# Kernel optimization log

Hardware: AMD Instinct MI355X
Metric: run time of the kernel (lower is better)

Reference implementation:

```python
import jax, jax.numpy as jnp
import numpy as np

D_MODEL = 1024
N_HEADS = 16


def setup_inputs() -> dict:
    key = jax.random.key(0)
    ks = jax.random.split(key, 5)
    B, L, D = 2, 2048, D_MODEL
    x = jax.random.normal(ks[0], (B, L, D), dtype=jnp.float32)
    # Linear params (torch nn.Linear: y = x @ W.T + b); store as (in, out) for einsum.
    s_attn = 1.0 / np.sqrt(D)
    W_attn = jax.random.uniform(ks[1], (D, 3 * D), jnp.float32, -s_attn, s_attn)
    b_attn = jax.random.uniform(ks[2], (3 * D,), jnp.float32, -s_attn, s_attn)
    W_proj = jax.random.uniform(ks[3], (D, D), jnp.float32, -s_attn, s_attn)
    b_proj = jax.random.uniform(ks[4], (D,), jnp.float32, -s_attn, s_attn)
    return {"x": x, "W_attn": W_attn, "b_attn": b_attn, "W_proj": W_proj, "b_proj": b_proj}


def reference(x, W_attn, b_attn, W_proj, b_proj):
    B, L, D = x.shape
    H = N_HEADS
    hd = D // H
    qkv = jnp.einsum('bld,de->ble', x, W_attn) + b_attn  # [B,L,3D]
    # Faithful to source bug: q and v are both taken from the k projection.
    k_lin = qkv[:, :, D:2 * D]
    k = k_lin.reshape(B, L, H, hd).transpose(0, 2, 1, 3)  # [B,H,L,hd]
    q = k
    v = k
    att = jnp.einsum('bhqd,bhkd->bhqk', q, k) / jnp.sqrt(jnp.float32(hd))
    att = jax.nn.softmax(att, axis=3)
    out = jnp.einsum('bhqk,bhkd->bhqd', att, v)  # [B,H,L,hd]
    out = out.transpose(0, 2, 1, 3).reshape(B, L, D)
    return jnp.einsum('bld,de->ble', out, W_proj) + b_proj
```

## Files before the change

### kernel.cpp

```cpp
#include <hip/hip_runtime.h>
#include <hip/hip_bf16.h>

typedef __attribute__((ext_vector_type(8))) short short8;
typedef __attribute__((ext_vector_type(4))) float f32x4;
typedef __attribute__((ext_vector_type(16))) float f32x16;
typedef unsigned short u16;
typedef unsigned int u32;

static __device__ __forceinline__ u16 f2b(float f) {
  __hip_bfloat16 h = __float2bfloat16(f);
  return __builtin_bit_cast(u16, h);
}
static __device__ __forceinline__ float b2f(u16 v) {
  return __builtin_bit_cast(float, ((u32)v) << 16);
}
static __device__ __forceinline__ u32 pk2(float lo, float hi) {
  return (u32)f2b(lo) | ((u32)f2b(hi) << 16);
}
static __device__ __forceinline__ u32 cvtpk(float lo, float hi) {
  u32 r;
  asm("v_cvt_pk_bf16_f32 %0, %1, %2" : "=v"(r) : "v"(lo), "v"(hi));
  return r;
}

static __device__ __forceinline__ void gload16(const void* g, void* l) {
  __builtin_amdgcn_global_load_lds((const __attribute__((address_space(1))) void*)g,
                                   (__attribute__((address_space(3))) void*)l, 16, 0, 0);
}

static __device__ __forceinline__ void barrier_fenced() {
  __builtin_amdgcn_sched_barrier(0);
  asm volatile("" ::: "memory");
  __builtin_amdgcn_s_barrier();
  __builtin_amdgcn_sched_barrier(0);
  asm volatile("" ::: "memory");
}

__global__ __launch_bounds__(256) void prep(const float4* __restrict__ x4,
                                            uint2* __restrict__ xb,
                                            const float* __restrict__ W_attn,
                                            u16* __restrict__ Wkt,
                                            const float* __restrict__ W_proj,
                                            u16* __restrict__ Wpt) {
  __shared__ u16 tile[32][33];
  int bid = blockIdx.x, t = threadIdx.x;
  if (bid < 4096) {
    int i = bid * 256 + t;
    float4 v = x4[i];
    uint2 o;
    o.x = pk2(v.x, v.y);
    o.y = pk2(v.z, v.w);
    xb[i] = o;
    return;
  }
  const float* in;
  u16* out;
  int in_rs, col_off, blk;
  if (bid < 5120) {
    in = W_attn; out = Wkt; in_rs = 3072; col_off = 1024; blk = bid - 4096;
  } else {
    in = W_proj; out = Wpt; in_rs = 1024; col_off = 0; blk = bid - 5120;
  }
  int tx = t & 31, ty = t >> 5;
  int r0 = (blk >> 5) * 32, c0 = (blk & 31) * 32;
#pragma unroll
  for (int i = 0; i < 4; ++i) {
    int r = r0 + ty + i * 8;
    tile[ty + i * 8][tx] = f2b(in[(size_t)r * in_rs + col_off + c0 + tx]);
  }
  __syncthreads();
#pragma unroll
  for (int i = 0; i < 4; ++i) {
    int c = c0 + ty + i * 8;
    out[(size_t)c * 1024 + r0 + tx] = tile[tx][ty + i * 8];
  }
}

__global__ __launch_bounds__(256) void transpose_heads(const u16* __restrict__ in,
                                                       u16* __restrict__ out) {
  __shared__ u16 tile[32][33];
  int t = threadIdx.x, tx = t & 31, ty = t >> 5;
  int r0 = (blockIdx.x >> 5) * 32;
  int c0 = (blockIdx.x & 31) * 32;
#pragma unroll
  for (int i = 0; i < 4; ++i)
    tile[ty + i * 8][tx] = in[(size_t)(r0 + ty + i * 8) * 1024 + c0 + tx];
  __syncthreads();
  int r = r0 + tx;
  int b = r >> 11;
#pragma unroll
  for (int i = 0; i < 4; ++i) {
    int c = c0 + ty + i * 8;
    out[((size_t)(b * 1024 + c) << 11) + (r & 2047)] = tile[tx][ty + i * 8];
  }
}

template <bool OUT_F32>
__global__ __launch_bounds__(256) void gemm_bias(const u16* __restrict__ A,
                                                 const u16* __restrict__ Bt,
                                                 const float* __restrict__ bias,
                                                 void* __restrict__ Cp, int M, int N, int K) {
  __shared__ char lds[3][24576];
  int tid = threadIdx.x, lane = tid & 63, wid = tid >> 6;
  int lr = lane & 15, lh = lane >> 4;
  int p = blockIdx.x;
  int m0 = (p >> 3) << 6, n0 = (p & 7) << 7;
  int wm = wid >> 1, wn = wid & 1;
  f32x4 acc[2][4] = {};
  int srow = lane >> 3;
  int scol = ((lane & 7) << 4) ^ (srow << 4);
  const char* Ab = (const char*)A;
  const char* Bb = (const char*)Bt;
  int r0 = wid * 8;
  const int NT = K >> 6;

  auto stage = [&](char* buf, int k0) {
    char* lA = buf;
    char* lB = buf + 8192;
    gload16(Ab + ((size_t)(m0 + r0 + srow) * K + k0) * 2 + scol, lA + r0 * 128);
    gload16(Ab + ((size_t)(m0 + 32 + r0 + srow) * K + k0) * 2 + scol, lA + (32 + r0) * 128);
#pragma unroll
    for (int i = 0; i < 4; ++i)
      gload16(Bb + ((size_t)(n0 + i * 32 + r0 + srow) * K + k0) * 2 + scol,
              lB + (i * 32 + r0) * 128);
  };

  stage(lds[0], 0);
  stage(lds[1], 64);
  for (int t = 0; t < NT; ++t) {
    if (t + 1 < NT)
      asm volatile("s_waitcnt vmcnt(6) lgkmcnt(0)" ::: "memory");
    else
      asm volatile("s_waitcnt vmcnt(0) lgkmcnt(0)" ::: "memory");
    barrier_fenced();
    char* lA = lds[t % 3];
    char* lB = lA + 8192;
    short8 af[2][2], bfr[4][2];
#pragma unroll
    for (int mi = 0; mi < 2; ++mi)
#pragma unroll
      for (int ks = 0; ks < 2; ++ks) {
        int row = wm * 32 + mi * 16 + lr;
        af[mi][ks] = *(const short8*)(lA + row * 128 + ((ks * 64 + lh * 16) ^ ((row & 7) << 4)));
      }
#pragma unroll
    for (int ni = 0; ni < 4; ++ni)
#pragma unroll
      for (int ks = 0; ks < 2; ++ks) {
        int row = wn * 64 + ni * 16 + lr;
        bfr[ni][ks] = *(const short8*)(lB + row * 128 + ((ks * 64 + lh * 16) ^ ((row & 7) << 4)));
      }
    __builtin_amdgcn_s_setprio(1);
#pragma unroll
    for (int ks = 0; ks < 2; ++ks)
#pragma unroll
      for (int mi = 0; mi < 2; ++mi)
#pragma unroll
        for (int ni = 0; ni < 4; ++ni)
          acc[mi][ni] = __builtin_amdgcn_mfma_f32_16x16x32_bf16(af[mi][ks], bfr[ni][ks],
                                                                acc[mi][ni], 0, 0, 0);
    __builtin_amdgcn_s_setprio(0);
    if (t + 2 < NT) stage(lds[(t + 2) % 3], (t + 2) << 6);
  }
#pragma unroll
  for (int mi = 0; mi < 2; ++mi)
#pragma unroll
    for (int ni = 0; ni < 4; ++ni) {
      int col = n0 + wn * 64 + ni * 16 + lr;
      float bz = bias[col];
#pragma unroll
      for (int r = 0; r < 4; ++r) {
        int row = m0 + wm * 32 + mi * 16 + lh * 4 + r;
        float v = acc[mi][ni][r] + bz;
        if (OUT_F32)
          ((float*)Cp)[(size_t)row * N + col] = v;
        else
          ((u16*)Cp)[(size_t)row * N + col] = f2b(v);
      }
    }
}

__global__ __launch_bounds__(256) void flash_attn(const u16* __restrict__ Kb,
                                                  const u16* __restrict__ Kt,
                                                  u16* __restrict__ AO) {
  __shared__ char kv[3][16384];
  const float S2 = 0.125f * 1.44269504088896340736f;
  int tid = threadIdx.x, lane = tid & 63, wid = tid >> 6;
  int ql = lane & 31, half = lane >> 5;
  int rb = blockIdx.x;
  int bid = (rb & 7) * 64 + (rb >> 3);
  int qb = bid & 15, h = (bid >> 4) & 15, b = bid >> 8;
  int qbase = b * 2048 + qb * 128 + wid * 32;
  int hc = h * 64;
  short8 qfr[4];
#pragma unroll
  for (int ds = 0; ds < 4; ++ds) {
    short8 raw = *(const short8*)(Kb + (size_t)(qbase + ql) * 1024 + hc + ds * 16 + half * 8);
    short8 q;
#pragma unroll
    for (int j = 0; j < 8; ++j) q[j] = (short)f2b(b2f((u16)raw[j]) * S2);
    qfr[ds] = q;
  }
  const short8 ones = {0x3F80, 0x3F80, 0x3F80, 0x3F80, 0x3F80, 0x3F80, 0x3F80, 0x3F80};
  f32x16 acc0 = {}, acc1 = {}, accs = {};
  int srow = lane >> 3;
  int scol = ((lane & 7) << 4) ^ (srow << 4);
  const char* Kbase = (const char*)Kb + (size_t)(b * 2048) * 2048 + hc * 2;
  const char* Vbase = (const char*)Kt + (size_t)((b * 16 + h) * 64) * 4096;

  auto stage = [&](char* buf, int kt) {
    const char* kp = Kbase + (size_t)(kt * 64) * 2048;
    const char* vp = Vbase + (size_t)(kt * 128);
    char* lk = buf;
    char* lv = buf + 8192;
#pragma unroll
    for (int j = 0; j < 2; ++j) {
      int row = wid * 8 + j * 32 + srow;
      gload16(kp + (size_t)row * 2048 + scol, lk + (wid * 8 + j * 32) * 128);
      gload16(vp + (size_t)row * 4096 + scol, lv + (wid * 8 + j * 32) * 128);
    }
  };

  stage(kv[0], 0);
  stage(kv[1], 1);
  for (int kt = 0; kt < 32; ++kt) {
    if (kt + 1 < 32)
      asm volatile("s_waitcnt vmcnt(4) lgkmcnt(0)" ::: "memory");
    else
      asm volatile("s_waitcnt vmcnt(0) lgkmcnt(0)" ::: "memory");
    barrier_fenced();
    const char* lk = kv[kt % 3];
    const char* lv = lk + 8192;
    short8 kf[2][4];
#pragma unroll
    for (int kb = 0; kb < 2; ++kb)
#pragma unroll
      for (int ds = 0; ds < 4; ++ds) {
        int row = kb * 32 + ql;
        kf[kb][ds] = *(const short8*)(lk + row * 128 + ((ds * 32 + half * 16) ^ ((row & 7) << 4)));
      }
    f32x16 s0 = {}, s1 = {};
    __builtin_amdgcn_s_setprio(1);
#pragma unroll
    for (int ds = 0; ds < 4; ++ds) {
      s0 = __builtin_amdgcn_mfma_f32_32x32x16_bf16(kf[0][ds], qfr[ds], s0, 0, 0, 0);
      s1 = __builtin_amdgcn_mfma_f32_32x32x16_bf16(kf[1][ds], qfr[ds], s1, 0, 0, 0);
    }
    __builtin_amdgcn_s_setprio(0);
    short8 vf0[4], vf1[4];
#pragma unroll
    for (int ks = 0; ks < 4; ++ks) {
      int row0 = ql, row1 = 32 + ql;
      vf0[ks] = *(const short8*)(lv + row0 * 128 + ((ks * 32 + half * 16) ^ ((row0 & 7) << 4)));
      vf1[ks] = *(const short8*)(lv + row1 * 128 + ((ks * 32 + half * 16) ^ ((row1 & 7) << 4)));
    }
    float p[32];
#pragma unroll
    for (int i = 0; i < 16; ++i) p[i] = __builtin_amdgcn_exp2f(s0[i]);
#pragma unroll
    for (int i = 0; i < 16; ++i) p[16 + i] = __builtin_amdgcn_exp2f(s1[i]);
    u32 w0[8], w1[8];
#pragma unroll
    for (int g = 0; g < 8; ++g) {
      int idx = (g >> 2) * 16 + (g & 3) * 4;
      w0[g] = cvtpk(p[idx], p[idx + 1]);
      w1[g] = cvtpk(p[idx + 2], p[idx + 3]);
    }
    short8 pa[4];
#pragma unroll
    for (int ks = 0; ks < 4; ++ks) {
      u32 a0 = w0[2 * ks], b0 = w0[2 * ks + 1];
      u32 a1 = w1[2 * ks], b1 = w1[2 * ks + 1];
      asm volatile("v_permlane32_swap_b32 %0, %1" : "+v"(a0), "+v"(b0));
      asm volatile("v_permlane32_swap_b32 %0, %1" : "+v"(a1), "+v"(b1));
      uint4 words = {a0, a1, b0, b1};
      pa[ks] = __builtin_bit_cast(short8, words);
    }
    __builtin_amdgcn_s_setprio(1);
#pragma unroll
    for (int ks = 0; ks < 4; ++ks) {
      acc0 = __builtin_amdgcn_mfma_f32_32x32x16_bf16(pa[ks], vf0[ks], acc0, 0, 0, 0);
      acc1 = __builtin_amdgcn_mfma_f32_32x32x16_bf16(pa[ks], vf1[ks], acc1, 0, 0, 0);
      accs = __builtin_amdgcn_mfma_f32_32x32x16_bf16(pa[ks], ones, accs, 0, 0, 0);
    }
    __builtin_amdgcn_s_setprio(0);
    if (kt + 2 < 32) stage(kv[(kt + 2) % 3], kt + 2);
  }
#pragma unroll
  for (int reg = 0; reg < 16; ++reg) {
    int ridx = (reg & 3) + 8 * (reg >> 2) + 4 * half;
    float iv = __builtin_amdgcn_rcpf(accs[reg]);
    int grow = qbase + ridx;
    AO[(size_t)grow * 1024 + hc + ql] = f2b(acc0[reg] * iv);
    AO[(size_t)grow * 1024 + hc + 32 + ql] = f2b(acc1[reg] * iv);
  }
}


extern "C" void kernel_launch(void* const* d_in, const int* in_sizes, int n_in, void* d_out,
                              int out_size, void* d_ws, size_t ws_size, hipStream_t stream) {
  const float* x = (const float*)d_in[0];
  const float* W_attn = (const float*)d_in[1];
  const float* b_attn = (const float*)d_in[2];
  const float* W_proj = (const float*)d_in[3];
  const float* b_proj = (const float*)d_in[4];
  float* out = (float*)d_out;
  char* ws = (char*)d_ws;
  u16* xb = (u16*)(ws);
  u16* Kb = (u16*)(ws + 8388608);
  u16* Kt = (u16*)(ws + 16777216);
  u16* Wkt = (u16*)(ws + 25165824);
  u16* Wpt = (u16*)(ws + 27262976);

  prep<<<6144, 256, 0, stream>>>((const float4*)x, (uint2*)xb, W_attn, Wkt, W_proj, Wpt);
  gemm_bias<false><<<512, 256, 0, stream>>>(xb, Wkt, b_attn + 1024, (void*)Kb, 4096, 1024, 1024);
  transpose_heads<<<4096, 256, 0, stream>>>(Kb, Kt);
  u16* AO = xb;
  flash_attn<<<512, 256, 0, stream>>>(Kb, Kt, AO);
  gemm_bias<true><<<512, 256, 0, stream>>>(AO, Wpt, b_proj, (void*)out, 4096, 1024, 1024);
}
```

Baseline: 95.77 us.

## Fuse K transpose into QKV GEMM epilogue and pair KV tiles in attention

The first GEMM epilogue now also writes a transposed copy of K (per batch, feature-major) with a 4-element vector store, so the separate transpose_heads kernel and its extra read and write of K are gone. The flash attention loop switches from a 3-slot single-tile pipeline to a double-buffered pair-of-tiles scheme: it loads two KV tiles per barrier and interleaves the second tile's QK MFMAs with the first tile's PV MFMAs. This halves the number of barriers but waits on vmcnt(0) each iteration, and LDS use rises from 48 KB to 64 KB, which may lower occupancy.

New measurement: 92.57 us. 1.03x faster.

```diff
diff --git a/kernel.cpp b/kernel.cpp
--- a/kernel.cpp
+++ b/kernel.cpp
@@ -76,30 +76,12 @@
   }
 }
 
-__global__ __launch_bounds__(256) void transpose_heads(const u16* __restrict__ in,
-                                                       u16* __restrict__ out) {
-  __shared__ u16 tile[32][33];
-  int t = threadIdx.x, tx = t & 31, ty = t >> 5;
-  int r0 = (blockIdx.x >> 5) * 32;
-  int c0 = (blockIdx.x & 31) * 32;
-#pragma unroll
-  for (int i = 0; i < 4; ++i)
-    tile[ty + i * 8][tx] = in[(size_t)(r0 + ty + i * 8) * 1024 + c0 + tx];
-  __syncthreads();
-  int r = r0 + tx;
-  int b = r >> 11;
-#pragma unroll
-  for (int i = 0; i < 4; ++i) {
-    int c = c0 + ty + i * 8;
-    out[((size_t)(b * 1024 + c) << 11) + (r & 2047)] = tile[tx][ty + i * 8];
-  }
-}
-
-template <bool OUT_F32>
+template <int MODE>
 __global__ __launch_bounds__(256) void gemm_bias(const u16* __restrict__ A,
                                                  const u16* __restrict__ Bt,
                                                  const float* __restrict__ bias,
-                                                 void* __restrict__ Cp, int M, int N, int K) {
+                                                 void* __restrict__ Cp, u16* __restrict__ Ktp,
+                                                 int M, int N, int K) {
   __shared__ char lds[3][24576];
   int tid = threadIdx.x, lane = tid & 63, wid = tid >> 6;
   int lr = lane & 15, lh = lane >> 4;
@@ -168,14 +150,21 @@
     for (int ni = 0; ni < 4; ++ni) {
       int col = n0 + wn * 64 + ni * 16 + lr;
       float bz = bias[col];
-#pragma unroll
-      for (int r = 0; r < 4; ++r) {
-        int row = m0 + wm * 32 + mi * 16 + lh * 4 + r;
-        float v = acc[mi][ni][r] + bz;
-        if (OUT_F32)
-          ((float*)Cp)[(size_t)row * N + col] = v;
-        else
-          ((u16*)Cp)[(size_t)row * N + col] = f2b(v);
+      int row0 = m0 + wm * 32 + mi * 16 + lh * 4;
+      if (MODE == 1) {
+#pragma unroll
+        for (int r = 0; r < 4; ++r)
+          ((float*)Cp)[(size_t)(row0 + r) * N + col] = acc[mi][ni][r] + bz;
+      } else {
+        ushort4 q;
+        u16* qa = (u16*)&q;
+#pragma unroll
+        for (int r = 0; r < 4; ++r) {
+          u16 v = f2b(acc[mi][ni][r] + bz);
+          qa[r] = v;
+          ((u16*)Cp)[(size_t)(row0 + r) * N + col] = v;
+        }
+        *(ushort4*)(Ktp + ((size_t)((row0 >> 11) * 1024 + col)) * 2048 + (row0 & 2047)) = q;
       }
     }
 }
@@ -183,7 +172,7 @@
 __global__ __launch_bounds__(256) void flash_attn(const u16* __restrict__ Kb,
                                                   const u16* __restrict__ Kt,
                                                   u16* __restrict__ AO) {
-  __shared__ char kv[3][16384];
+  __shared__ char kv[2][32768];
   const float S2 = 0.125f * 1.44269504088896340736f;
   int tid = threadIdx.x, lane = tid & 63, wid = tid >> 6;
   int ql = lane & 31, half = lane >> 5;
@@ -208,30 +197,24 @@
   const char* Kbase = (const char*)Kb + (size_t)(b * 2048) * 2048 + hc * 2;
   const char* Vbase = (const char*)Kt + (size_t)((b * 16 + h) * 64) * 4096;
 
-  auto stage = [&](char* buf, int kt) {
-    const char* kp = Kbase + (size_t)(kt * 64) * 2048;
-    const char* vp = Vbase + (size_t)(kt * 128);
-    char* lk = buf;
-    char* lv = buf + 8192;
-#pragma unroll
-    for (int j = 0; j < 2; ++j) {
-      int row = wid * 8 + j * 32 + srow;
-      gload16(kp + (size_t)row * 2048 + scol, lk + (wid * 8 + j * 32) * 128);
-      gload16(vp + (size_t)row * 4096 + scol, lv + (wid * 8 + j * 32) * 128);
-    }
-  };
-
-  stage(kv[0], 0);
-  stage(kv[1], 1);
-  for (int kt = 0; kt < 32; ++kt) {
-    if (kt + 1 < 32)
-      asm volatile("s_waitcnt vmcnt(4) lgkmcnt(0)" ::: "memory");
-    else
-      asm volatile("s_waitcnt vmcnt(0) lgkmcnt(0)" ::: "memory");
-    barrier_fenced();
-    const char* lk = kv[kt % 3];
-    const char* lv = lk + 8192;
-    short8 kf[2][4];
+  auto stage_pair = [&](char* buf, int pt) {
+#pragma unroll
+    for (int tt = 0; tt < 2; ++tt) {
+      int kt = 2 * pt + tt;
+      const char* kp = Kbase + (size_t)(kt * 64) * 2048;
+      const char* vp = Vbase + (size_t)(kt * 128);
+      char* lk = buf + tt * 16384;
+      char* lv = lk + 8192;
+#pragma unroll
+      for (int j = 0; j < 2; ++j) {
+        int row = wid * 8 + j * 32 + srow;
+        gload16(kp + (size_t)row * 2048 + scol, lk + (wid * 8 + j * 32) * 128);
+        gload16(vp + (size_t)row * 4096 + scol, lv + (wid * 8 + j * 32) * 128);
+      }
+    }
+  };
+
+  auto read_kf = [&](const char* lk, short8 kf[2][4]) {
 #pragma unroll
     for (int kb = 0; kb < 2; ++kb)
 #pragma unroll
@@ -239,21 +222,16 @@
         int row = kb * 32 + ql;
         kf[kb][ds] = *(const short8*)(lk + row * 128 + ((ds * 32 + half * 16) ^ ((row & 7) << 4)));
       }
-    f32x16 s0 = {}, s1 = {};
-    __builtin_amdgcn_s_setprio(1);
-#pragma unroll
-    for (int ds = 0; ds < 4; ++ds) {
-      s0 = __builtin_amdgcn_mfma_f32_32x32x16_bf16(kf[0][ds], qfr[ds], s0, 0, 0, 0);
-      s1 = __builtin_amdgcn_mfma_f32_32x32x16_bf16(kf[1][ds], qfr[ds], s1, 0, 0, 0);
-    }
-    __builtin_amdgcn_s_setprio(0);
-    short8 vf0[4], vf1[4];
+  };
+  auto read_vf = [&](const char* lv, short8 vf0[4], short8 vf1[4]) {
 #pragma unroll
     for (int ks = 0; ks < 4; ++ks) {
       int row0 = ql, row1 = 32 + ql;
       vf0[ks] = *(const short8*)(lv + row0 * 128 + ((ks * 32 + half * 16) ^ ((row0 & 7) << 4)));
       vf1[ks] = *(const short8*)(lv + row1 * 128 + ((ks * 32 + half * 16) ^ ((row1 & 7) << 4)));
     }
+  };
+  auto softmax_pack = [&](const f32x16& s0, const f32x16& s1, short8 pa[4]) {
     float p[32];
 #pragma unroll
     for (int i = 0; i < 16; ++i) p[i] = __builtin_amdgcn_exp2f(s0[i]);
@@ -266,7 +244,6 @@
       w0[g] = cvtpk(p[idx], p[idx + 1]);
       w1[g] = cvtpk(p[idx + 2], p[idx + 3]);
     }
-    short8 pa[4];
 #pragma unroll
     for (int ks = 0; ks < 4; ++ks) {
       u32 a0 = w0[2 * ks], b0 = w0[2 * ks + 1];
@@ -276,15 +253,61 @@
       uint4 words = {a0, a1, b0, b1};
       pa[ks] = __builtin_bit_cast(short8, words);
     }
+  };
+
+  stage_pair(kv[0], 0);
+  for (int pt = 0; pt < 16; ++pt) {
+    asm volatile("s_waitcnt vmcnt(0) lgkmcnt(0)" ::: "memory");
+    barrier_fenced();
+    if (pt + 1 < 16) stage_pair(kv[(pt + 1) & 1], pt + 1);
+    const char* lkA = kv[pt & 1];
+    const char* lvA = lkA + 8192;
+    const char* lkB = lkA + 16384;
+    const char* lvB = lkB + 8192;
+    short8 kfA[2][4];
+    read_kf(lkA, kfA);
+    f32x16 s0 = {}, s1 = {};
+    __builtin_amdgcn_s_setprio(1);
+#pragma unroll
+    for (int ds = 0; ds < 4; ++ds) {
+      s0 = __builtin_amdgcn_mfma_f32_32x32x16_bf16(kfA[0][ds], qfr[ds], s0, 0, 0, 0);
+      s1 = __builtin_amdgcn_mfma_f32_32x32x16_bf16(kfA[1][ds], qfr[ds], s1, 0, 0, 0);
+    }
+    __builtin_amdgcn_s_setprio(0);
+    short8 vfA0[4], vfA1[4];
+    read_vf(lvA, vfA0, vfA1);
+    short8 paA[4];
+    softmax_pack(s0, s1, paA);
+    short8 kfB[2][4];
+    read_kf(lkB, kfB);
     __builtin_amdgcn_s_setprio(1);
 #pragma unroll
     for (int ks = 0; ks < 4; ++ks) {
-      acc0 = __builtin_amdgcn_mfma_f32_32x32x16_bf16(pa[ks], vf0[ks], acc0, 0, 0, 0);
-      acc1 = __builtin_amdgcn_mfma_f32_32x32x16_bf16(pa[ks], vf1[ks], acc1, 0, 0, 0);
-      accs = __builtin_amdgcn_mfma_f32_32x32x16_bf16(pa[ks], ones, accs, 0, 0, 0);
-    }
-    __builtin_amdgcn_s_setprio(0);
-    if (kt + 2 < 32) stage(kv[(kt + 2) % 3], kt + 2);
+      acc0 = __builtin_amdgcn_mfma_f32_32x32x16_bf16(paA[ks], vfA0[ks], acc0, 0, 0, 0);
+      acc1 = __builtin_amdgcn_mfma_f32_32x32x16_bf16(paA[ks], vfA1[ks], acc1, 0, 0, 0);
+      accs = __builtin_amdgcn_mfma_f32_32x32x16_bf16(paA[ks], ones, accs, 0, 0, 0);
+    }
+    __builtin_amdgcn_s_setprio(0);
+    f32x16 t0 = {}, t1 = {};
+    __builtin_amdgcn_s_setprio(1);
+#pragma unroll
+    for (int ds = 0; ds < 4; ++ds) {
+      t0 = __builtin_amdgcn_mfma_f32_32x32x16_bf16(kfB[0][ds], qfr[ds], t0, 0, 0, 0);
+      t1 = __builtin_amdgcn_mfma_f32_32x32x16_bf16(kfB[1][ds], qfr[ds], t1, 0, 0, 0);
+    }
+    __builtin_amdgcn_s_setprio(0);
+    short8 vfB0[4], vfB1[4];
+    read_vf(lvB, vfB0, vfB1);
+    short8 paB[4];
+    softmax_pack(t0, t1, paB);
+    __builtin_amdgcn_s_setprio(1);
+#pragma unroll
+    for (int ks = 0; ks < 4; ++ks) {
+      acc0 = __builtin_amdgcn_mfma_f32_32x32x16_bf16(paB[ks], vfB0[ks], acc0, 0, 0, 0);
+      acc1 = __builtin_amdgcn_mfma_f32_32x32x16_bf16(paB[ks], vfB1[ks], acc1, 0, 0, 0);
+      accs = __builtin_amdgcn_mfma_f32_32x32x16_bf16(paB[ks], ones, accs, 0, 0, 0);
+    }
+    __builtin_amdgcn_s_setprio(0);
   }
 #pragma unroll
   for (int reg = 0; reg < 16; ++reg) {
@@ -313,9 +336,8 @@
   u16* Wpt = (u16*)(ws + 27262976);
 
   prep<<<6144, 256, 0, stream>>>((const float4*)x, (uint2*)xb, W_attn, Wkt, W_proj, Wpt);
-  gemm_bias<false><<<512, 256, 0, stream>>>(xb, Wkt, b_attn + 1024, (void*)Kb, 4096, 1024, 1024);
-  transpose_heads<<<4096, 256, 0, stream>>>(Kb, Kt);
+  gemm_bias<0><<<512, 256, 0, stream>>>(xb, Wkt, b_attn + 1024, (void*)Kb, Kt, 4096, 1024, 1024);
   u16* AO = xb;
   flash_attn<<<512, 256, 0, stream>>>(Kb, Kt, AO);
-  gemm_bias<true><<<512, 256, 0, stream>>>(AO, Wpt, b_proj, (void*)out, 4096, 1024, 1024);
-}
+  gemm_bias<1><<<512, 256, 0, stream>>>(AO, Wpt, b_proj, (void*)out, nullptr, 4096, 1024, 1024);
+}
```

## Fuse head transpose into GEMM epilogue and shrink flash-attention blocks

Applied to the files above, without the earlier changes.

The separate transpose kernel is removed; the QKV GEMM epilogue now also writes the transposed K layout with 4-element vector stores. The flash attention kernel moves to 128-thread blocks covering 64 queries each, doubles the grid, and switches from triple to double buffering with the next tile issued after the barrier. This cuts a launch and a full read/write pass of K, and may raise occupancy. The risks are poorly coalesced transposed stores, halved K/V reuse per block, and less load/compute overlap from waiting on vmcnt(0) every iteration.

Result: slower. 100.6 us (+5.0%).

```diff
diff --git a/kernel.cpp b/kernel.cpp
--- a/kernel.cpp
+++ b/kernel.cpp
@@ -76,30 +76,12 @@
   }
 }
 
-__global__ __launch_bounds__(256) void transpose_heads(const u16* __restrict__ in,
-                                                       u16* __restrict__ out) {
-  __shared__ u16 tile[32][33];
-  int t = threadIdx.x, tx = t & 31, ty = t >> 5;
-  int r0 = (blockIdx.x >> 5) * 32;
-  int c0 = (blockIdx.x & 31) * 32;
-#pragma unroll
-  for (int i = 0; i < 4; ++i)
-    tile[ty + i * 8][tx] = in[(size_t)(r0 + ty + i * 8) * 1024 + c0 + tx];
-  __syncthreads();
-  int r = r0 + tx;
-  int b = r >> 11;
-#pragma unroll
-  for (int i = 0; i < 4; ++i) {
-    int c = c0 + ty + i * 8;
-    out[((size_t)(b * 1024 + c) << 11) + (r & 2047)] = tile[tx][ty + i * 8];
-  }
-}
-
-template <bool OUT_F32>
+template <int MODE>
 __global__ __launch_bounds__(256) void gemm_bias(const u16* __restrict__ A,
                                                  const u16* __restrict__ Bt,
                                                  const float* __restrict__ bias,
-                                                 void* __restrict__ Cp, int M, int N, int K) {
+                                                 void* __restrict__ Cp, u16* __restrict__ Ktp,
+                                                 int M, int N, int K) {
   __shared__ char lds[3][24576];
   int tid = threadIdx.x, lane = tid & 63, wid = tid >> 6;
   int lr = lane & 15, lh = lane >> 4;
@@ -168,29 +150,36 @@
     for (int ni = 0; ni < 4; ++ni) {
       int col = n0 + wn * 64 + ni * 16 + lr;
       float bz = bias[col];
-#pragma unroll
-      for (int r = 0; r < 4; ++r) {
-        int row = m0 + wm * 32 + mi * 16 + lh * 4 + r;
-        float v = acc[mi][ni][r] + bz;
-        if (OUT_F32)
-          ((float*)Cp)[(size_t)row * N + col] = v;
-        else
-          ((u16*)Cp)[(size_t)row * N + col] = f2b(v);
+      int row0 = m0 + wm * 32 + mi * 16 + lh * 4;
+      if (MODE == 1) {
+#pragma unroll
+        for (int r = 0; r < 4; ++r)
+          ((float*)Cp)[(size_t)(row0 + r) * N + col] = acc[mi][ni][r] + bz;
+      } else {
+        ushort4 q;
+        u16* qa = (u16*)&q;
+#pragma unroll
+        for (int r = 0; r < 4; ++r) {
+          u16 v = f2b(acc[mi][ni][r] + bz);
+          qa[r] = v;
+          ((u16*)Cp)[(size_t)(row0 + r) * N + col] = v;
+        }
+        *(ushort4*)(Ktp + ((size_t)((row0 >> 11) * 1024 + col)) * 2048 + (row0 & 2047)) = q;
       }
     }
 }
 
-__global__ __launch_bounds__(256) void flash_attn(const u16* __restrict__ Kb,
+__global__ __launch_bounds__(128) void flash_attn(const u16* __restrict__ Kb,
                                                   const u16* __restrict__ Kt,
                                                   u16* __restrict__ AO) {
-  __shared__ char kv[3][16384];
+  __shared__ char kv[2][16384];
   const float S2 = 0.125f * 1.44269504088896340736f;
   int tid = threadIdx.x, lane = tid & 63, wid = tid >> 6;
   int ql = lane & 31, half = lane >> 5;
   int rb = blockIdx.x;
-  int bid = (rb & 7) * 64 + (rb >> 3);
-  int qb = bid & 15, h = (bid >> 4) & 15, b = bid >> 8;
-  int qbase = b * 2048 + qb * 128 + wid * 32;
+  int bid = (rb & 7) * 128 + (rb >> 3);
+  int qt = bid & 31, h = (bid >> 5) & 15, b = bid >> 9;
+  int qbase = b * 2048 + qt * 64 + wid * 32;
   int hc = h * 64;
   short8 qfr[4];
 #pragma unroll
@@ -214,22 +203,20 @@
     char* lk = buf;
     char* lv = buf + 8192;
 #pragma unroll
-    for (int j = 0; j < 2; ++j) {
-      int row = wid * 8 + j * 32 + srow;
-      gload16(kp + (size_t)row * 2048 + scol, lk + (wid * 8 + j * 32) * 128);
-      gload16(vp + (size_t)row * 4096 + scol, lv + (wid * 8 + j * 32) * 128);
+    for (int j = 0; j < 4; ++j) {
+      int grp = j * 2 + wid;
+      int row = grp * 8 + srow;
+      gload16(kp + (size_t)row * 2048 + scol, lk + grp * 8 * 128);
+      gload16(vp + (size_t)row * 4096 + scol, lv + grp * 8 * 128);
     }
   };
 
   stage(kv[0], 0);
-  stage(kv[1], 1);
   for (int kt = 0; kt < 32; ++kt) {
-    if (kt + 1 < 32)
-      asm volatile("s_waitcnt vmcnt(4) lgkmcnt(0)" ::: "memory");
-    else
-      asm volatile("s_waitcnt vmcnt(0) lgkmcnt(0)" ::: "memory");
+    asm volatile("s_waitcnt vmcnt(0) lgkmcnt(0)" ::: "memory");
     barrier_fenced();
-    const char* lk = kv[kt % 3];
+    if (kt + 1 < 32) stage(kv[(kt + 1) & 1], kt + 1);
+    const char* lk = kv[kt & 1];
     const char* lv = lk + 8192;
     short8 kf[2][4];
 #pragma unroll
@@ -284,7 +271,6 @@
       accs = __builtin_amdgcn_mfma_f32_32x32x16_bf16(pa[ks], ones, accs, 0, 0, 0);
     }
     __builtin_amdgcn_s_setprio(0);
-    if (kt + 2 < 32) stage(kv[(kt + 2) % 3], kt + 2);
   }
 #pragma unroll
   for (int reg = 0; reg < 16; ++reg) {
@@ -313,9 +299,8 @@
   u16* Wpt = (u16*)(ws + 27262976);
 
   prep<<<6144, 256, 0, stream>>>((const float4*)x, (uint2*)xb, W_attn, Wkt, W_proj, Wpt);
-  gemm_bias<false><<<512, 256, 0, stream>>>(xb, Wkt, b_attn + 1024, (void*)Kb, 4096, 1024, 1024);
-  transpose_heads<<<4096, 256, 0, stream>>>(Kb, Kt);
+  gemm_bias<0><<<512, 256, 0, stream>>>(xb, Wkt, b_attn + 1024, (void*)Kb, Kt, 4096, 1024, 1024);
   u16* AO = xb;
-  flash_attn<<<512, 256, 0, stream>>>(Kb, Kt, AO);
-  gemm_bias<true><<<512, 256, 0, stream>>>(AO, Wpt, b_proj, (void*)out, 4096, 1024, 1024);
-}
+  flash_attn<<<1024, 128, 0, stream>>>(Kb, Kt, AO);
+  gemm_bias<1><<<512, 256, 0, stream>>>(AO, Wpt, b_proj, (void*)out, nullptr, 4096, 1024, 1024);
+}
```
